# Optimization experiments

Measured on AMD Instinct MI355X. Metric: run time of the kernel, lower is better.

The kernel has to match this reference:

```python
import jax, jax.numpy as jnp
import numpy as np


def setup_inputs() -> dict:
    key = jax.random.key(0)
    kq, kk, kv = jax.random.split(key, 3)
    B, H, S, D = 1, 16, 4096, 64
    Q = jax.random.normal(kq, (B, H, S, D), dtype=jnp.float32)
    K = jax.random.normal(kk, (B, H, S, D), dtype=jnp.float32)
    V = jax.random.normal(kv, (B, H, S, D), dtype=jnp.float32)
    return {"Q": Q, "K": K, "V": V}


def reference(Q, K, V):
    # scores: [B, H, len_q, len_k], scaled by sqrt(dim_k)
    dim_k = K.shape[-1]
    scale = 1.0 / jnp.sqrt(jnp.asarray(dim_k, dtype=Q.dtype))
    scores = jnp.einsum("bhqd,bhkd->bhqk", Q, K) * scale
    attention = jax.nn.softmax(scores, axis=-1)
    context = jnp.einsum("bhqk,bhkd->bhqd", attention, V)
    return context
```

## Files before the change

kernel.cpp:

```cpp
#include <hip/hip_runtime.h>
#include <hip/hip_bf16.h>

typedef short bf16x8 __attribute__((ext_vector_type(8)));
typedef __bf16 bfv8  __attribute__((ext_vector_type(8)));
typedef float f32x4  __attribute__((ext_vector_type(4)));

#define S_LEN 4096
#define DDIM  64
#define KVB   32
#define QBLK  128
#define NHEAD 16
#define THR   7.0f

#define MFMA(a, b, c) __builtin_amdgcn_mfma_f32_16x16x32_bf16((a), (b), (c), 0, 0, 0)

static __device__ __forceinline__ float exp2v(float x) {
    return __builtin_amdgcn_exp2f(x);
}

static __device__ __forceinline__ unsigned pk2t(float lo, float hi) {
    return __builtin_amdgcn_perm(__builtin_bit_cast(unsigned, hi),
                                 __builtin_bit_cast(unsigned, lo), 0x07060302u);
}

static __device__ __forceinline__ int4 cvt8(float4 a, float4 b) {
    bfv8 r;
    r[0] = (__bf16)a.x; r[1] = (__bf16)a.y; r[2] = (__bf16)a.z; r[3] = (__bf16)a.w;
    r[4] = (__bf16)b.x; r[5] = (__bf16)b.y; r[6] = (__bf16)b.z; r[7] = (__bf16)b.w;
    return __builtin_bit_cast(int4, r);
}

static __device__ __forceinline__ bf16x8 ldfrag(const unsigned char* base, int row, int doff) {
    int addr = (row * 128 + doff * 2) ^ ((row & 7) << 4);
    return *reinterpret_cast<const bf16x8*>(base + addr);
}

static __device__ __forceinline__ void stage(unsigned char* base, int swaddr,
                                             float4 a, float4 b, float4 c, float4 d) {
    *reinterpret_cast<int4*>(base + swaddr)        = cvt8(a, b);
    *reinterpret_cast<int4*>(base + 4096 + swaddr) = cvt8(c, d);
}

static __device__ __forceinline__ void sm_pv(f32x4 s0, f32x4 s1, float& m,
                                             f32x4 acc[4], f32x4& lacc,
                                             const bf16x8 vf[4], bf16x8 ones) {
    float mx = fmaxf(fmaxf(fmaxf(s0[0], s0[1]), s0[2]),
                     fmaxf(fmaxf(s0[3], s1[0]),
                           fmaxf(s1[1], fmaxf(s1[2], s1[3]))));
    if (!__all(mx <= m + THR)) {
        float pm = fmaxf(mx, __shfl_xor(mx, 16));
        pm = fmaxf(pm, __shfl_xor(pm, 32));
        float mn = fmaxf(m, pm);
        float al = exp2v(m - mn);
        #pragma unroll
        for (int dk = 0; dk < 4; ++dk)
            #pragma unroll
            for (int j = 0; j < 4; ++j) acc[dk][j] *= al;
        #pragma unroll
        for (int j = 0; j < 4; ++j) lacc[j] *= al;
        m = mn;
    }
    float p[8];
    #pragma unroll
    for (int j = 0; j < 4; ++j) p[j]     = exp2v(s0[j] - m);
    #pragma unroll
    for (int j = 0; j < 4; ++j) p[4 + j] = exp2v(s1[j] - m);
    bfv8 r;
    #pragma unroll
    for (int j = 0; j < 8; ++j) r[j] = (__bf16)p[j];
    bf16x8 pb = __builtin_bit_cast(bf16x8, r);
    lacc = MFMA(ones, pb, lacc);
    #pragma unroll
    for (int dk = 0; dk < 4; ++dk) acc[dk] = MFMA(vf[dk], pb, acc[dk]);
}

template <int KSPLIT>
__global__ __launch_bounds__(256, 3) void attn_fwd(
    const float* __restrict__ Qg, const float* __restrict__ Kg,
    const float* __restrict__ Vg, float* __restrict__ Og,
    float* __restrict__ wsO, float* __restrict__ wsML)
{
    const int h    = blockIdx.y;
    const int qb   = blockIdx.x;
    const int ks   = (KSPLIT > 1) ? blockIdx.z : 0;
    const int NT   = (S_LEN / KVB) / KSPLIT;
    const int tid  = threadIdx.x;
    const int lane = tid & 63;
    const int wv   = tid >> 6;
    const int g    = lane >> 4;
    const int r16  = lane & 15;

    __shared__ __align__(16) unsigned char lds[16384];

    const float QSC = 0.125f * 1.44269504088896f;
    const int qrow0 = qb * QBLK + wv * 32 + r16;
    bf16x8 qf0[2], qf1[2];
    {
        const float* qp0 = Qg + ((size_t)h * S_LEN + qrow0) * DDIM;
        const float* qp1 = qp0 + 16 * DDIM;
        #pragma unroll
        for (int c = 0; c < 2; ++c) {
            float4 x = *reinterpret_cast<const float4*>(qp0 + 32 * c + 8 * g);
            float4 y = *reinterpret_cast<const float4*>(qp0 + 32 * c + 8 * g + 4);
            float4 xs = {x.x * QSC, x.y * QSC, x.z * QSC, x.w * QSC};
            float4 ys = {y.x * QSC, y.y * QSC, y.z * QSC, y.w * QSC};
            qf0[c] = __builtin_bit_cast(bf16x8, cvt8(xs, ys));
            x = *reinterpret_cast<const float4*>(qp1 + 32 * c + 8 * g);
            y = *reinterpret_cast<const float4*>(qp1 + 32 * c + 8 * g + 4);
            xs = {x.x * QSC, x.y * QSC, x.z * QSC, x.w * QSC};
            ys = {y.x * QSC, y.y * QSC, y.z * QSC, y.w * QSC};
            qf1[c] = __builtin_bit_cast(bf16x8, cvt8(xs, ys));
        }
    }

    bf16x8 idf[2];
    #pragma unroll
    for (int c2 = 0; c2 < 2; ++c2) {
        #pragma unroll
        for (int e = 0; e < 8; ++e) {
            bool on = ((g >> 1) == c2) && ((r16 >> 3) == (g & 1)) && (e == (r16 & 7));
            idf[c2][e] = on ? (short)0x3F80 : (short)0;
        }
    }
    bf16x8 ones;
    #pragma unroll
    for (int e = 0; e < 8; ++e) ones[e] = (short)0x3F80;

    const int srow   = tid >> 3;
    const int sd     = (tid & 7) * 8;
    const int swaddr = (srow * 128 + sd * 2) ^ ((srow & 7) << 4);
    const size_t kvoff = (size_t)h * S_LEN * DDIM
                       + (size_t)ks * (S_LEN / KSPLIT) * DDIM
                       + (size_t)srow * DDIM + sd;
    const float* kp = Kg + kvoff;
    const float* vp = Vg + kvoff;

    float4 ka = *reinterpret_cast<const float4*>(kp);
    float4 kb = *reinterpret_cast<const float4*>(kp + 4);
    float4 va = *reinterpret_cast<const float4*>(vp);
    float4 vb = *reinterpret_cast<const float4*>(vp + 4);
    stage(lds, swaddr, ka, kb, va, vb);
    kp += KVB * DDIM; vp += KVB * DDIM;
    ka = *reinterpret_cast<const float4*>(kp);
    kb = *reinterpret_cast<const float4*>(kp + 4);
    va = *reinterpret_cast<const float4*>(vp);
    vb = *reinterpret_cast<const float4*>(vp + 4);
    __syncthreads();

    const f32x4 z0 = {0.f, 0.f, 0.f, 0.f};
    f32x4 accA[4] = {z0, z0, z0, z0};
    f32x4 accB[4] = {z0, z0, z0, z0};
    f32x4 laccA = z0, laccB = z0;
    float m0 = -INFINITY, m1 = -INFINITY;

    int c = 0;
    for (int kt = 0; kt < NT; ++kt) {
        const unsigned char* Klds = lds + c * 8192;
        const unsigned char* Vlds = lds + c * 8192 + 4096;

        if (kt + 1 < NT) {
            stage(lds + (c ^ 1) * 8192, swaddr, ka, kb, va, vb);
            if (kt + 2 < NT) {
                kp += KVB * DDIM; vp += KVB * DDIM;
                ka = *reinterpret_cast<const float4*>(kp);
                kb = *reinterpret_cast<const float4*>(kp + 4);
                va = *reinterpret_cast<const float4*>(vp);
                vb = *reinterpret_cast<const float4*>(vp + 4);
            }
        }

        f32x4 sA0 = z0, sA1 = z0, sB0 = z0, sB1 = z0;
        #pragma unroll
        for (int cc = 0; cc < 2; ++cc) {
            bf16x8 k0 = ldfrag(Klds, r16,      32 * cc + 8 * g);
            bf16x8 k1 = ldfrag(Klds, 16 + r16, 32 * cc + 8 * g);
            sA0 = MFMA(k0, qf0[cc], sA0);
            sA1 = MFMA(k1, qf0[cc], sA1);
            sB0 = MFMA(k0, qf1[cc], sB0);
            sB1 = MFMA(k1, qf1[cc], sB1);
        }

        bf16x8 vf[4];
        #pragma unroll
        for (int dc = 0; dc < 2; ++dc) {
            bf16x8 av0 = ldfrag(Vlds, r16,      32 * dc + 8 * g);
            bf16x8 av1 = ldfrag(Vlds, 16 + r16, 32 * dc + 8 * g);
            #pragma unroll
            for (int ci = 0; ci < 2; ++ci) {
                f32x4 t0 = MFMA(av0, idf[ci], z0);
                f32x4 t1 = MFMA(av1, idf[ci], z0);
                int4 w;
                w.x = (int)pk2t(t0[0], t0[1]); w.y = (int)pk2t(t0[2], t0[3]);
                w.z = (int)pk2t(t1[0], t1[1]); w.w = (int)pk2t(t1[2], t1[3]);
                vf[2 * dc + ci] = __builtin_bit_cast(bf16x8, w);
            }
        }

        sm_pv(sA0, sA1, m0, accA, laccA, vf, ones);
        sm_pv(sB0, sB1, m1, accB, laccB, vf, ones);

        __syncthreads();
        c ^= 1;
    }

    if (KSPLIT == 1) {
        float inv0 = 1.0f / laccA[0];
        float* op = Og + ((size_t)h * S_LEN + qrow0) * DDIM;
        #pragma unroll
        for (int dk = 0; dk < 4; ++dk) {
            float4 o = {accA[dk][0] * inv0, accA[dk][1] * inv0,
                        accA[dk][2] * inv0, accA[dk][3] * inv0};
            *reinterpret_cast<float4*>(op + 16 * dk + 4 * g) = o;
        }
        float inv1 = 1.0f / laccB[0];
        op += 16 * DDIM;
        #pragma unroll
        for (int dk = 0; dk < 4; ++dk) {
            float4 o = {accB[dk][0] * inv1, accB[dk][1] * inv1,
                        accB[dk][2] * inv1, accB[dk][3] * inv1};
            *reinterpret_cast<float4*>(op + 16 * dk + 4 * g) = o;
        }
    } else {
        const size_t R0 = (size_t)h * S_LEN + qrow0;
        float* o0 = wsO + ((size_t)ks * (NHEAD * S_LEN) + R0) * DDIM;
        #pragma unroll
        for (int dk = 0; dk < 4; ++dk) {
            float4 o = {accA[dk][0], accA[dk][1], accA[dk][2], accA[dk][3]};
            *reinterpret_cast<float4*>(o0 + 16 * dk + 4 * g) = o;
        }
        o0 += 16 * DDIM;
        #pragma unroll
        for (int dk = 0; dk < 4; ++dk) {
            float4 o = {accB[dk][0], accB[dk][1], accB[dk][2], accB[dk][3]};
            *reinterpret_cast<float4*>(o0 + 16 * dk + 4 * g) = o;
        }
        if (g == 0) {
            float2 v0 = {m0, laccA[0]};
            float2 v1 = {m1, laccB[0]};
            *reinterpret_cast<float2*>(wsML + ((size_t)ks * (NHEAD * S_LEN) + R0) * 2)      = v0;
            *reinterpret_cast<float2*>(wsML + ((size_t)ks * (NHEAD * S_LEN) + R0 + 16) * 2) = v1;
        }
    }
}

__global__ __launch_bounds__(256) void combine2(
    const float* __restrict__ wsO, const float* __restrict__ wsML,
    float* __restrict__ Og)
{
    const int NR = NHEAD * S_LEN;
    int t  = blockIdx.x * 256 + threadIdx.x;
    int R  = t >> 4;
    int d4 = (t & 15) * 4;
    float2 ml0 = *reinterpret_cast<const float2*>(wsML + (size_t)R * 2);
    float2 ml1 = *reinterpret_cast<const float2*>(wsML + ((size_t)NR + R) * 2);
    float m  = fmaxf(ml0.x, ml1.x);
    float a0 = exp2v(ml0.x - m);
    float a1 = exp2v(ml1.x - m);
    float inv = 1.0f / (a0 * ml0.y + a1 * ml1.y);
    a0 *= inv; a1 *= inv;
    float4 o0 = *reinterpret_cast<const float4*>(wsO + (size_t)R * DDIM + d4);
    float4 o1 = *reinterpret_cast<const float4*>(wsO + ((size_t)NR + R) * DDIM + d4);
    float4 o = {a0 * o0.x + a1 * o1.x, a0 * o0.y + a1 * o1.y,
                a0 * o0.z + a1 * o1.z, a0 * o0.w + a1 * o1.w};
    *reinterpret_cast<float4*>(Og + (size_t)R * DDIM + d4) = o;
}

extern "C" void kernel_launch(void* const* d_in, const int* in_sizes, int n_in,
                              void* d_out, int out_size, void* d_ws, size_t ws_size,
                              hipStream_t stream) {
    const float* Q = (const float*)d_in[0];
    const float* K = (const float*)d_in[1];
    const float* V = (const float*)d_in[2];
    float* O = (float*)d_out;

    const size_t nO  = (size_t)2 * NHEAD * S_LEN * DDIM;
    const size_t nML = (size_t)2 * NHEAD * S_LEN * 2;
    const size_t need = (nO + nML) * sizeof(float);

    if (ws_size >= need) {
        float* wsO  = (float*)d_ws;
        float* wsML = wsO + nO;
        dim3 grid(S_LEN / QBLK, NHEAD, 2);
        attn_fwd<2><<<grid, dim3(256, 1, 1), 0, stream>>>(Q, K, V, O, wsO, wsML);
        int nthr = NHEAD * S_LEN * (DDIM / 4);
        combine2<<<dim3(nthr / 256), dim3(256, 1, 1), 0, stream>>>(wsO, wsML, O);
    } else {
        dim3 grid(S_LEN / QBLK, NHEAD, 1);
        attn_fwd<1><<<grid, dim3(256, 1, 1), 0, stream>>>(Q, K, V, O, nullptr, nullptr);
    }
}
```

Measured before the change: 124.3 us.

## Pre-transpose V to bf16 in a separate kernel and store split partials in bf16

Adds a transpose_v kernel that converts V to bf16 once and lays it out transposed in the key-permuted order the PV MFMA expects. The main loop then loads V fragments straight from padded LDS instead of transposing them per tile with identity MFMAs. The split-K partial outputs are also written and read as bf16 instead of fp32, halving that workspace traffic. The cost is an extra kernel launch plus a full pass over V, lower precision in the partials, and a path that writes no output when the workspace is too small.

```diff
diff --git a/kernel.cpp b/kernel.cpp
--- a/kernel.cpp
+++ b/kernel.cpp
@@ -3,6 +3,7 @@
 
 typedef short bf16x8 __attribute__((ext_vector_type(8)));
 typedef __bf16 bfv8  __attribute__((ext_vector_type(8)));
+typedef __bf16 bfv4  __attribute__((ext_vector_type(4)));
 typedef float f32x4  __attribute__((ext_vector_type(4)));
 
 #define S_LEN 4096
@@ -11,16 +12,13 @@
 #define QBLK  128
 #define NHEAD 16
 #define THR   7.0f
+#define VOFFB 4096
+#define BUFSZ 9216
 
 #define MFMA(a, b, c) __builtin_amdgcn_mfma_f32_16x16x32_bf16((a), (b), (c), 0, 0, 0)
 
 static __device__ __forceinline__ float exp2v(float x) {
     return __builtin_amdgcn_exp2f(x);
-}
-
-static __device__ __forceinline__ unsigned pk2t(float lo, float hi) {
-    return __builtin_amdgcn_perm(__builtin_bit_cast(unsigned, hi),
-                                 __builtin_bit_cast(unsigned, lo), 0x07060302u);
 }
 
 static __device__ __forceinline__ int4 cvt8(float4 a, float4 b) {
@@ -29,21 +27,25 @@
     r[4] = (__bf16)b.x; r[5] = (__bf16)b.y; r[6] = (__bf16)b.z; r[7] = (__bf16)b.w;
     return __builtin_bit_cast(int4, r);
 }
+static __device__ __forceinline__ int2 cvt4(f32x4 a) {
+    bfv4 r;
+    r[0] = (__bf16)a[0]; r[1] = (__bf16)a[1]; r[2] = (__bf16)a[2]; r[3] = (__bf16)a[3];
+    return __builtin_bit_cast(int2, r);
+}
 
 static __device__ __forceinline__ bf16x8 ldfrag(const unsigned char* base, int row, int doff) {
     int addr = (row * 128 + doff * 2) ^ ((row & 7) << 4);
     return *reinterpret_cast<const bf16x8*>(base + addr);
 }
 
-static __device__ __forceinline__ void stage(unsigned char* base, int swaddr,
-                                             float4 a, float4 b, float4 c, float4 d) {
-    *reinterpret_cast<int4*>(base + swaddr)        = cvt8(a, b);
-    *reinterpret_cast<int4*>(base + 4096 + swaddr) = cvt8(c, d);
-}
-
-static __device__ __forceinline__ void sm_pv(f32x4 s0, f32x4 s1, float& m,
-                                             f32x4 acc[4], f32x4& lacc,
-                                             const bf16x8 vf[4], bf16x8 ones) {
+static __device__ __forceinline__ void stage(unsigned char* base, int swK, int swV,
+                                             float4 ka, float4 kb, int4 vt) {
+    *reinterpret_cast<int4*>(base + swK)         = cvt8(ka, kb);
+    *reinterpret_cast<int4*>(base + VOFFB + swV) = vt;
+}
+
+static __device__ __forceinline__ bf16x8 softmax_pb(f32x4 s0, f32x4 s1, float& m,
+                                                    f32x4 acc[4], f32x4& lacc) {
     float mx = fmaxf(fmaxf(fmaxf(s0[0], s0[1]), s0[2]),
                      fmaxf(fmaxf(s0[3], s1[0]),
                            fmaxf(s1[1], fmaxf(s1[2], s1[3]))));
@@ -60,25 +62,55 @@
         for (int j = 0; j < 4; ++j) lacc[j] *= al;
         m = mn;
     }
-    float p[8];
-    #pragma unroll
-    for (int j = 0; j < 4; ++j) p[j]     = exp2v(s0[j] - m);
-    #pragma unroll
-    for (int j = 0; j < 4; ++j) p[4 + j] = exp2v(s1[j] - m);
     bfv8 r;
     #pragma unroll
-    for (int j = 0; j < 8; ++j) r[j] = (__bf16)p[j];
-    bf16x8 pb = __builtin_bit_cast(bf16x8, r);
-    lacc = MFMA(ones, pb, lacc);
-    #pragma unroll
-    for (int dk = 0; dk < 4; ++dk) acc[dk] = MFMA(vf[dk], pb, acc[dk]);
+    for (int j = 0; j < 4; ++j) {
+        r[2 * j]     = (__bf16)exp2v(s0[j] - m);
+        r[2 * j + 1] = (__bf16)exp2v(s1[j] - m);
+    }
+    return __builtin_bit_cast(bf16x8, r);
+}
+
+__global__ __launch_bounds__(256) void transpose_v(
+    const float* __restrict__ Vg, unsigned short* __restrict__ wsVT)
+{
+    const int h  = blockIdx.y;
+    const int kt = blockIdx.x;
+    const int t  = threadIdx.x;
+    __shared__ __align__(16) unsigned short vt[32][68];
+
+    {
+        const int key = t >> 3;
+        const int d0  = (t & 7) * 8;
+        const float* vp = Vg + (((size_t)h * S_LEN) + (size_t)kt * 32 + key) * DDIM + d0;
+        float4 a = *reinterpret_cast<const float4*>(vp);
+        float4 b = *reinterpret_cast<const float4*>(vp + 4);
+        int4 w = cvt8(a, b);
+        int2 lo = {w.x, w.y}, hi = {w.z, w.w};
+        *reinterpret_cast<int2*>(&vt[key][d0])     = lo;
+        *reinterpret_cast<int2*>(&vt[key][d0 + 4]) = hi;
+    }
+    __syncthreads();
+    {
+        const int d  = t >> 2;
+        const int p0 = (t & 3) * 8;
+        unsigned short out[8];
+        #pragma unroll
+        for (int i = 0; i < 8; ++i) {
+            int p   = p0 + i;
+            int key = 4 * (p >> 3) + ((p & 7) >> 1) + 16 * (p & 1);
+            out[i] = vt[key][d];
+        }
+        size_t off = (((size_t)h * DDIM + d) * 128 + kt) * 32 + p0;
+        *reinterpret_cast<int4*>(wsVT + off) = *reinterpret_cast<const int4*>(out);
+    }
 }
 
 template <int KSPLIT>
 __global__ __launch_bounds__(256, 3) void attn_fwd(
     const float* __restrict__ Qg, const float* __restrict__ Kg,
-    const float* __restrict__ Vg, float* __restrict__ Og,
-    float* __restrict__ wsO, float* __restrict__ wsML)
+    const unsigned short* __restrict__ wsVT, float* __restrict__ Og,
+    unsigned short* __restrict__ wsO, float* __restrict__ wsML)
 {
     const int h    = blockIdx.y;
     const int qb   = blockIdx.x;
@@ -90,7 +122,7 @@
     const int g    = lane >> 4;
     const int r16  = lane & 15;
 
-    __shared__ __align__(16) unsigned char lds[16384];
+    __shared__ __align__(16) unsigned char lds[2 * BUFSZ];
 
     const float QSC = 0.125f * 1.44269504088896f;
     const int qrow0 = qb * QBLK + wv * 32 + r16;
@@ -113,38 +145,31 @@
         }
     }
 
-    bf16x8 idf[2];
-    #pragma unroll
-    for (int c2 = 0; c2 < 2; ++c2) {
-        #pragma unroll
-        for (int e = 0; e < 8; ++e) {
-            bool on = ((g >> 1) == c2) && ((r16 >> 3) == (g & 1)) && (e == (r16 & 7));
-            idf[c2][e] = on ? (short)0x3F80 : (short)0;
-        }
-    }
     bf16x8 ones;
     #pragma unroll
     for (int e = 0; e < 8; ++e) ones[e] = (short)0x3F80;
 
-    const int srow   = tid >> 3;
-    const int sd     = (tid & 7) * 8;
-    const int swaddr = (srow * 128 + sd * 2) ^ ((srow & 7) << 4);
-    const size_t kvoff = (size_t)h * S_LEN * DDIM
-                       + (size_t)ks * (S_LEN / KSPLIT) * DDIM
-                       + (size_t)srow * DDIM + sd;
-    const float* kp = Kg + kvoff;
-    const float* vp = Vg + kvoff;
+    const int srow = tid >> 3;
+    const int sd   = (tid & 7) * 8;
+    const int swK  = (srow * 128 + sd * 2) ^ ((srow & 7) << 4);
+    const int vrow = tid >> 2;
+    const int swV  = vrow * 80 + (tid & 3) * 16;
+
+    const float* kp = Kg + (size_t)h * S_LEN * DDIM
+                    + (size_t)ks * (S_LEN / KSPLIT) * DDIM
+                    + (size_t)srow * DDIM + sd;
+    const unsigned short* vtp = wsVT
+        + (((size_t)h * DDIM + vrow) * 128 + (size_t)ks * (128 / KSPLIT)) * 32
+        + (tid & 3) * 8;
 
     float4 ka = *reinterpret_cast<const float4*>(kp);
     float4 kb = *reinterpret_cast<const float4*>(kp + 4);
-    float4 va = *reinterpret_cast<const float4*>(vp);
-    float4 vb = *reinterpret_cast<const float4*>(vp + 4);
-    stage(lds, swaddr, ka, kb, va, vb);
-    kp += KVB * DDIM; vp += KVB * DDIM;
+    int4   vt = *reinterpret_cast<const int4*>(vtp);
+    stage(lds, swK, swV, ka, kb, vt);
+    kp += KVB * DDIM; vtp += 32;
     ka = *reinterpret_cast<const float4*>(kp);
     kb = *reinterpret_cast<const float4*>(kp + 4);
-    va = *reinterpret_cast<const float4*>(vp);
-    vb = *reinterpret_cast<const float4*>(vp + 4);
+    vt = *reinterpret_cast<const int4*>(vtp);
     __syncthreads();
 
     const f32x4 z0 = {0.f, 0.f, 0.f, 0.f};
@@ -155,18 +180,25 @@
 
     int c = 0;
     for (int kt = 0; kt < NT; ++kt) {
-        const unsigned char* Klds = lds + c * 8192;
-        const unsigned char* Vlds = lds + c * 8192 + 4096;
+        const unsigned char* Klds = lds + c * BUFSZ;
+        const unsigned char* Vlds = Klds + VOFFB;
 
         if (kt + 1 < NT) {
-            stage(lds + (c ^ 1) * 8192, swaddr, ka, kb, va, vb);
+            stage(lds + (c ^ 1) * BUFSZ, swK, swV, ka, kb, vt);
             if (kt + 2 < NT) {
-                kp += KVB * DDIM; vp += KVB * DDIM;
+                kp += KVB * DDIM; vtp += 32;
                 ka = *reinterpret_cast<const float4*>(kp);
                 kb = *reinterpret_cast<const float4*>(kp + 4);
-                va = *reinterpret_cast<const float4*>(vp);
-                vb = *reinterpret_cast<const float4*>(vp + 4);
+                vt = *reinterpret_cast<const int4*>(vtp);
             }
+        }
+
+        bf16x8 vf[4];
+        {
+            const unsigned char* vbase = Vlds + r16 * 80 + 16 * g;
+            #pragma unroll
+            for (int dk = 0; dk < 4; ++dk)
+                vf[dk] = *reinterpret_cast<const bf16x8*>(vbase + dk * 1280);
         }
 
         f32x4 sA0 = z0, sA1 = z0, sB0 = z0, sB1 = z0;
@@ -180,24 +212,15 @@
             sB1 = MFMA(k1, qf1[cc], sB1);
         }
 
-        bf16x8 vf[4];
-        #pragma unroll
-        for (int dc = 0; dc < 2; ++dc) {
-            bf16x8 av0 = ldfrag(Vlds, r16,      32 * dc + 8 * g);
-            bf16x8 av1 = ldfrag(Vlds, 16 + r16, 32 * dc + 8 * g);
-            #pragma unroll
-            for (int ci = 0; ci < 2; ++ci) {
-                f32x4 t0 = MFMA(av0, idf[ci], z0);
-                f32x4 t1 = MFMA(av1, idf[ci], z0);
-                int4 w;
-                w.x = (int)pk2t(t0[0], t0[1]); w.y = (int)pk2t(t0[2], t0[3]);
-                w.z = (int)pk2t(t1[0], t1[1]); w.w = (int)pk2t(t1[2], t1[3]);
-                vf[2 * dc + ci] = __builtin_bit_cast(bf16x8, w);
-            }
-        }
-
-        sm_pv(sA0, sA1, m0, accA, laccA, vf, ones);
-        sm_pv(sB0, sB1, m1, accB, laccB, vf, ones);
+        bf16x8 pbA = softmax_pb(sA0, sA1, m0, accA, laccA);
+        bf16x8 pbB = softmax_pb(sB0, sB1, m1, accB, laccB);
+
+        laccA = MFMA(ones, pbA, laccA);
+        #pragma unroll
+        for (int dk = 0; dk < 4; ++dk) accA[dk] = MFMA(vf[dk], pbA, accA[dk]);
+        laccB = MFMA(ones, pbB, laccB);
+        #pragma unroll
+        for (int dk = 0; dk < 4; ++dk) accB[dk] = MFMA(vf[dk], pbB, accB[dk]);
 
         __syncthreads();
         c ^= 1;
@@ -222,18 +245,14 @@
         }
     } else {
         const size_t R0 = (size_t)h * S_LEN + qrow0;
-        float* o0 = wsO + ((size_t)ks * (NHEAD * S_LEN) + R0) * DDIM;
-        #pragma unroll
-        for (int dk = 0; dk < 4; ++dk) {
-            float4 o = {accA[dk][0], accA[dk][1], accA[dk][2], accA[dk][3]};
-            *reinterpret_cast<float4*>(o0 + 16 * dk + 4 * g) = o;
-        }
+        unsigned short* o0 = wsO + ((size_t)ks * (NHEAD * S_LEN) + R0) * DDIM;
+        #pragma unroll
+        for (int dk = 0; dk < 4; ++dk)
+            *reinterpret_cast<int2*>(o0 + 16 * dk + 4 * g) = cvt4(accA[dk]);
         o0 += 16 * DDIM;
         #pragma unroll
-        for (int dk = 0; dk < 4; ++dk) {
-            float4 o = {accB[dk][0], accB[dk][1], accB[dk][2], accB[dk][3]};
-            *reinterpret_cast<float4*>(o0 + 16 * dk + 4 * g) = o;
-        }
+        for (int dk = 0; dk < 4; ++dk)
+            *reinterpret_cast<int2*>(o0 + 16 * dk + 4 * g) = cvt4(accB[dk]);
         if (g == 0) {
             float2 v0 = {m0, laccA[0]};
             float2 v1 = {m1, laccB[0]};
@@ -244,7 +263,7 @@
 }
 
 __global__ __launch_bounds__(256) void combine2(
-    const float* __restrict__ wsO, const float* __restrict__ wsML,
+    const unsigned short* __restrict__ wsO, const float* __restrict__ wsML,
     float* __restrict__ Og)
 {
     const int NR = NHEAD * S_LEN;
@@ -258,10 +277,14 @@
     float a1 = exp2v(ml1.x - m);
     float inv = 1.0f / (a0 * ml0.y + a1 * ml1.y);
     a0 *= inv; a1 *= inv;
-    float4 o0 = *reinterpret_cast<const float4*>(wsO + (size_t)R * DDIM + d4);
-    float4 o1 = *reinterpret_cast<const float4*>(wsO + ((size_t)NR + R) * DDIM + d4);
-    float4 o = {a0 * o0.x + a1 * o1.x, a0 * o0.y + a1 * o1.y,
-                a0 * o0.z + a1 * o1.z, a0 * o0.w + a1 * o1.w};
+    bfv4 o0 = __builtin_bit_cast(bfv4,
+        *reinterpret_cast<const int2*>(wsO + (size_t)R * DDIM + d4));
+    bfv4 o1 = __builtin_bit_cast(bfv4,
+        *reinterpret_cast<const int2*>(wsO + ((size_t)NR + R) * DDIM + d4));
+    float4 o = {a0 * (float)o0[0] + a1 * (float)o1[0],
+                a0 * (float)o0[1] + a1 * (float)o1[1],
+                a0 * (float)o0[2] + a1 * (float)o1[2],
+                a0 * (float)o0[3] + a1 * (float)o1[3]};
     *reinterpret_cast<float4*>(Og + (size_t)R * DDIM + d4) = o;
 }
 
@@ -273,19 +296,24 @@
     const float* V = (const float*)d_in[2];
     float* O = (float*)d_out;
 
+    const size_t nVT = (size_t)NHEAD * DDIM * S_LEN;
     const size_t nO  = (size_t)2 * NHEAD * S_LEN * DDIM;
     const size_t nML = (size_t)2 * NHEAD * S_LEN * 2;
-    const size_t need = (nO + nML) * sizeof(float);
-
-    if (ws_size >= need) {
-        float* wsO  = (float*)d_ws;
-        float* wsML = wsO + nO;
+    const size_t needVT   = nVT * 2;
+    const size_t needFull = nVT * 2 + nO * 2 + nML * 4;
+
+    unsigned short* wsVT = (unsigned short*)d_ws;
+    transpose_v<<<dim3(128, NHEAD), dim3(256, 1, 1), 0, stream>>>(V, wsVT);
+
+    if (ws_size >= needFull) {
+        unsigned short* wsO  = wsVT + nVT;
+        float*          wsML = (float*)(wsO + nO);
         dim3 grid(S_LEN / QBLK, NHEAD, 2);
-        attn_fwd<2><<<grid, dim3(256, 1, 1), 0, stream>>>(Q, K, V, O, wsO, wsML);
+        attn_fwd<2><<<grid, dim3(256, 1, 1), 0, stream>>>(Q, K, wsVT, O, wsO, wsML);
         int nthr = NHEAD * S_LEN * (DDIM / 4);
         combine2<<<dim3(nthr / 256), dim3(256, 1, 1), 0, stream>>>(wsO, wsML, O);
-    } else {
+    } else if (ws_size >= needVT) {
         dim3 grid(S_LEN / QBLK, NHEAD, 1);
-        attn_fwd<1><<<grid, dim3(256, 1, 1), 0, stream>>>(Q, K, V, O, nullptr, nullptr);
-    }
-}
+        attn_fwd<1><<<grid, dim3(256, 1, 1), 0, stream>>>(Q, K, wsVT, O, nullptr, nullptr);
+    }
+}
```

Measured after the change: 102.7 us. 1.21x faster.
